# Performance work log

Measured on AMD Instinct MI355X. Metric: run time of the kernel, lower is better.

Reference implementation:

```python
import jax, jax.numpy as jnp
import numpy as np

D = 1024       # d_model
H = 16         # nhead
HD = D // H    # head_dim = 64
FF = 4096      # dim_feedforward
EPS = 1e-5


def layer_norm(x, gamma, beta, eps=EPS):
    mu = jnp.mean(x, axis=-1, keepdims=True)
    var = jnp.var(x, axis=-1, keepdims=True)
    return (x - mu) * jax.lax.rsqrt(var + eps) * gamma + beta


def setup_inputs() -> dict:
    key = jax.random.key(0)
    ks = jax.random.split(key, 12)
    rn = lambda k, shape, s=0.02: (jax.random.normal(k, shape, jnp.float32) * s)
    return {
        "src": jax.random.normal(ks[0], (4, 2048, D), jnp.float32),
        "Wqkv": rn(ks[1], (D, 3 * D)),          # qkv_proj weight (bias=False), stored (in,out)
        "Wout": rn(ks[2], (D, D)),              # out_proj weight (bias=False)
        "W1": rn(ks[3], (D, FF)),               # linear1
        "b1": jnp.zeros((FF,), jnp.float32),
        "W2": rn(ks[4], (FF, D)),               # linear2
        "b2": jnp.zeros((D,), jnp.float32),
        "g1": jnp.ones((D,), jnp.float32),      # norm1 weight
        "be1": jnp.zeros((D,), jnp.float32),    # norm1 bias
        "g2": jnp.ones((D,), jnp.float32),      # norm2 weight
        "be2": jnp.zeros((D,), jnp.float32),    # norm2 bias
    }


def reference(src, Wqkv, Wout, W1, b1, W2, b2, g1, be1, g2, be2):
    B, S, _ = src.shape
    # --- self attention (naive/MATH-backend SDPA, post-norm, eval: dropout=0) ---
    qkv = src @ Wqkv                                  # [B,S,3D]
    qkv = qkv.reshape(B, S, 3, H, HD)
    q = qkv[:, :, 0].transpose(0, 2, 1, 3)            # [B,H,S,HD]
    k = qkv[:, :, 1].transpose(0, 2, 1, 3)
    v = qkv[:, :, 2].transpose(0, 2, 1, 3)
    scores = jnp.einsum("bhqd,bhkd->bhqk", q, k) / np.float32(np.sqrt(HD))  # [B,H,S,S]
    attn = jax.nn.softmax(scores, axis=-1)
    ctx = jnp.einsum("bhqk,bhkd->bhqd", attn, v)      # [B,H,S,HD]
    ctx = ctx.transpose(0, 2, 1, 3).reshape(B, S, D)  # [B,S,D]
    attn_out = ctx @ Wout
    # residual + norm1
    x = layer_norm(src + attn_out, g1, be1)
    # --- FFN ---
    ff = jax.nn.relu(x @ W1 + b1) @ W2 + b2
    # residual + norm2
    return layer_norm(x + ff, g2, be2)
```

## Files before the change

### kernel.cpp

```cpp
#include <hip/hip_runtime.h>
#include <hip/hip_bf16.h>


typedef __attribute__((ext_vector_type(8))) short          short8;
typedef __attribute__((ext_vector_type(8))) unsigned short ushort8;
typedef __attribute__((ext_vector_type(4))) float          f32x4;
typedef __attribute__((ext_vector_type(2))) unsigned int   uivec2;

__device__ __forceinline__ unsigned short f2bf(float f) {
    union { float f; unsigned int u; } v; v.f = f;
    unsigned int u = v.u;
    unsigned int r = (u + 0x7fffu + ((u >> 16) & 1u)) >> 16;
    return (unsigned short)r;
}

__device__ __forceinline__ float bf2f(unsigned short u) {
    union { unsigned int u; float f; } v; v.u = ((unsigned int)u) << 16;
    return v.f;
}

__device__ __forceinline__ unsigned int pack_bf16_trunc(float lo, float hi) {
    union { float f; unsigned int u; } a, b; a.f = lo; b.f = hi;
    return __builtin_amdgcn_perm(b.u, a.u, 0x07060302u);
}

__device__ __forceinline__ void async_load16(const void* g, void* l) {
    __builtin_amdgcn_global_load_lds(
        (const __attribute__((address_space(1))) void*)(unsigned long long)g,
        (__attribute__((address_space(3))) void*)(unsigned long long)l,
        16, 0, 0);
}

__device__ __forceinline__ void softmax_frag(const f32x4* s,
                                             short8& pf0, short8& pf1) {
    unsigned int aw[4], bw[4];
#pragma unroll
    for (int nt = 0; nt < 4; nt++) {
        float p0 = __builtin_amdgcn_exp2f(s[nt][0]);
        float p1 = __builtin_amdgcn_exp2f(s[nt][1]);
        float p2 = __builtin_amdgcn_exp2f(s[nt][2]);
        float p3 = __builtin_amdgcn_exp2f(s[nt][3]);
        aw[nt] = pack_bf16_trunc(p0, p1);
        bw[nt] = pack_bf16_trunc(p2, p3);
    }
    uivec2 rA = __builtin_amdgcn_permlane32_swap(aw[0], aw[1], false, false);
    uivec2 sA = __builtin_amdgcn_permlane32_swap(aw[2], aw[3], false, false);
    uivec2 rB = __builtin_amdgcn_permlane32_swap(bw[0], bw[1], false, false);
    uivec2 sB = __builtin_amdgcn_permlane32_swap(bw[2], bw[3], false, false);
    uivec2 tA = __builtin_amdgcn_permlane16_swap(rA.x, rA.y, false, false);
    uivec2 uA = __builtin_amdgcn_permlane16_swap(sA.x, sA.y, false, false);
    uivec2 tB = __builtin_amdgcn_permlane16_swap(rB.x, rB.y, false, false);
    uivec2 uB = __builtin_amdgcn_permlane16_swap(sB.x, sB.y, false, false);
    union { unsigned int w[4]; short8 v; } P0, P1;
    P0.w[0] = tA.x; P0.w[1] = tB.x; P0.w[2] = tA.y; P0.w[3] = tB.y;
    P1.w[0] = uA.x; P1.w[1] = uB.x; P1.w[2] = uA.y; P1.w[3] = uB.y;
    pf0 = P0.v;
    pf1 = P1.v;
}

__device__ __forceinline__ void transpose_tile32(
    const float* __restrict__ W, unsigned short* __restrict__ Wt,
    int K, int N, int n0, int k0, float (*tile)[33]) {
    int tx = threadIdx.x & 31, ty = threadIdx.x >> 5;
#pragma unroll
    for (int i = 0; i < 32; i += 8)
        tile[ty + i][tx] = W[(size_t)(k0 + ty + i) * N + n0 + tx];
    __syncthreads();
#pragma unroll
    for (int i = 0; i < 32; i += 8)
        Wt[(size_t)(n0 + ty + i) * K + k0 + tx] = f2bf(tile[tx][ty + i]);
}

__global__ __launch_bounds__(256) void prep_kernel(
    const float* __restrict__ src, unsigned short* __restrict__ src_bf,
    const float* __restrict__ Wqkv, unsigned short* __restrict__ Wqkv_t,
    const float* __restrict__ Wout, unsigned short* __restrict__ Wout_t,
    const float* __restrict__ W1, unsigned short* __restrict__ W1_t,
    const float* __restrict__ W2, unsigned short* __restrict__ W2_t) {
    __shared__ float tile[32][33];
    const int bid = blockIdx.x;
    if (bid < 8192) {
        size_t i = ((size_t)bid * 256 + threadIdx.x) * 4;
        float4 v = *(const float4*)(src + i);
        ushort4 o;
        o.x = f2bf(v.x); o.y = f2bf(v.y); o.z = f2bf(v.z); o.w = f2bf(v.w);
        *(ushort4*)(src_bf + i) = o;
    } else if (bid < 11264) {
        int r = bid - 8192;
        transpose_tile32(Wqkv, Wqkv_t, 1024, 3072, (r % 96) * 32, (r / 96) * 32, tile);
    } else if (bid < 12288) {
        int r = bid - 11264;
        transpose_tile32(Wout, Wout_t, 1024, 1024, (r % 32) * 32, (r / 32) * 32, tile);
    } else if (bid < 16384) {
        int r = bid - 12288;
        transpose_tile32(W1, W1_t, 1024, 4096, (r % 128) * 32, (r / 128) * 32, tile);
    } else {
        int r = bid - 16384;
        transpose_tile32(W2, W2_t, 4096, 1024, (r % 32) * 32, (r / 32) * 32, tile);
    }
}

template <int MODE>
__global__ __launch_bounds__(256) void gemm_bf16_kernel(
    const unsigned short* __restrict__ A, const unsigned short* __restrict__ Bt,
    int M, int N, int K, int Kstride,
    float* __restrict__ outF, unsigned short* __restrict__ outB,
    const float* __restrict__ bias,
    const float* __restrict__ resF, const unsigned short* __restrict__ resB,
    unsigned short* __restrict__ vtB) {
    __shared__ unsigned short As[2][128 * 32];
    __shared__ unsigned short Bs[2][128 * 32];

    const int t = threadIdx.x;
    const int m0 = blockIdx.x * 128, n0 = blockIdx.y * 128;
    const int koff = blockIdx.z * K;
    const int wid = t >> 6, lane = t & 63;
    const int wm = wid >> 1, wn = wid & 1;
    const int lr = lane & 15, quad = lane >> 4;

    const int srow = lane >> 2;
    const int sch  = ((lane & 3) ^ (srow & 3)) * 8;
    const unsigned short* Ag =
        A  + (size_t)(m0 + wid * 32 + srow) * Kstride + koff + sch;
    const unsigned short* Bg =
        Bt + (size_t)(n0 + wid * 32 + srow) * Kstride + koff + sch;
    const int wofs = (wid * 32) * 32;
    const size_t rstep = (size_t)16 * Kstride;

    const int axs = ((quad ^ (lr & 3))) * 8;
    f32x4 acc[4][4] = {};

    const int nK = K >> 5;
    async_load16(Ag,         &As[0][wofs]);
    async_load16(Ag + rstep, &As[0][wofs + 16 * 32]);
    async_load16(Bg,         &Bs[0][wofs]);
    async_load16(Bg + rstep, &Bs[0][wofs + 16 * 32]);

    for (int kt = 0; kt < nK; kt++) {
        const int cur = kt & 1, nxt = cur ^ 1;
        __syncthreads();
        if (kt + 1 < nK) {
            const int k1 = (kt + 1) * 32;
            async_load16(Ag + k1,         &As[nxt][wofs]);
            async_load16(Ag + k1 + rstep, &As[nxt][wofs + 16 * 32]);
            async_load16(Bg + k1,         &Bs[nxt][wofs]);
            async_load16(Bg + k1 + rstep, &Bs[nxt][wofs + 16 * 32]);
        }

        short8 af[4], bfr[4];
#pragma unroll
        for (int i = 0; i < 4; i++) {
            af[i]  = *(const short8*)&As[cur][(wm * 64 + i * 16 + lr) * 32 + axs];
            bfr[i] = *(const short8*)&Bs[cur][(wn * 64 + i * 16 + lr) * 32 + axs];
        }
#pragma unroll
        for (int mi = 0; mi < 4; mi++)
#pragma unroll
            for (int ni = 0; ni < 4; ni++)
                acc[mi][ni] = __builtin_amdgcn_mfma_f32_16x16x32_bf16(
                    af[mi], bfr[ni], acc[mi][ni], 0, 0, 0);
    }

    const float QSC = 0.18033688011112042f;
#pragma unroll
    for (int mi = 0; mi < 4; mi++)
#pragma unroll
        for (int ni = 0; ni < 4; ni++) {
            const int col  = n0 + wn * 64 + ni * 16 + lr;
            const int row0 = m0 + wm * 64 + mi * 16 + quad * 4;
            if (MODE == 4 && col >= 2048) {
                int bb = row0 >> 11, ss = row0 & 2047, c = col - 2048;
                ushort4 ov;
                ov.x = f2bf(acc[mi][ni][0]); ov.y = f2bf(acc[mi][ni][1]);
                ov.z = f2bf(acc[mi][ni][2]); ov.w = f2bf(acc[mi][ni][3]);
                *(ushort4*)&vtB[((size_t)bb * 1024 + c) * 2048 + ss] = ov;
            } else {
#pragma unroll
                for (int r = 0; r < 4; r++) {
                    size_t idx = (size_t)(row0 + r) * N + col;
                    float v = acc[mi][ni][r];
                    if (MODE == 4) {
                        outB[idx] = f2bf(col < 1024 ? v * QSC : v);
                    } else if (MODE == 0) {
                        outB[idx] = f2bf(v);
                    } else if (MODE == 1) {
                        outF[idx] = v + resF[idx];
                    } else if (MODE == 2) {
                        v += bias[col];
                        outB[idx] = f2bf(v > 0.f ? v : 0.f);
                    } else if (MODE == 7) {
                        outB[idx] = f2bf(v + bf2f(resB[idx]));
                    } else if (MODE == 9) {
                        outB[idx] = f2bf(v + bias[col] + bf2f(resB[idx]));
                    }
                }
            }
        }
}

__global__ __launch_bounds__(256, 2) void attention_kernel(
    const unsigned short* __restrict__ qkv, const unsigned short* __restrict__ Vt,
    unsigned short* __restrict__ ctx) {
    __shared__ unsigned short Kbuf[2][64 * 64];
    __shared__ unsigned short Vbuf[2][64 * 64];

    const int qt = blockIdx.x, h = blockIdx.y, b = blockIdx.z;
    const int t = threadIdx.x, wid = t >> 6, lane = t & 63;
    const int lr = lane & 15, quad = lane >> 4;
    const int q0 = qt * 256 + wid * 64;

    short8 qf[4][2];
#pragma unroll
    for (int f = 0; f < 4; f++) {
        size_t qb = ((size_t)(b * 2048 + q0 + f * 16 + lr)) * 3072 + h * 64;
        qf[f][0] = *(const short8*)(qkv + qb + quad * 8);
        qf[f][1] = *(const short8*)(qkv + qb + 32 + quad * 8);
    }

    const int srow = wid * 8 + (lane >> 3);
    const int sch  = ((lane & 7) ^ (srow & 7)) * 8;
    const unsigned short* Kg =
        qkv + (size_t)b * 2048 * 3072 + 1024 + h * 64 + (size_t)srow * 3072 + sch;
    const unsigned short* Vg =
        Vt + ((size_t)b * 1024 + h * 64 + srow) * 2048 + sch;
    unsigned short* KsB = (unsigned short*)&Kbuf[0][(wid * 8) * 64];
    unsigned short* VsB = (unsigned short*)&Vbuf[0][(wid * 8) * 64];
    const int bufstep = 64 * 64;

    short8 ones;
#pragma unroll
    for (int i = 0; i < 8; i++) ones[i] = (short)0x3F80;

    f32x4 o[4][4] = {};
    f32x4 lacc[4] = {};

#pragma unroll
    for (int half = 0; half < 2; half++) {
        async_load16(Kg + (size_t)(half * 32) * 3072, KsB + half * 32 * 64);
        async_load16(Vg + (size_t)(half * 32) * 2048, VsB + half * 32 * 64);
    }

    const int swz = lr & 7;

    for (int kt = 0; kt < 32; kt++) {
        const int cur = kt & 1, nxt = cur ^ 1;
        __syncthreads();
        if (kt + 1 < 32) {
#pragma unroll
            for (int half = 0; half < 2; half++) {
                async_load16(Kg + (size_t)((kt + 1) * 64 + half * 32) * 3072,
                             KsB + nxt * bufstep + half * 32 * 64);
                async_load16(Vg + (size_t)(half * 32) * 2048 + (kt + 1) * 64,
                             VsB + nxt * bufstep + half * 32 * 64);
            }
        }

        const unsigned short* Kc = &Kbuf[cur][0];
        const unsigned short* Vc = &Vbuf[cur][0];

        f32x4 s[4][4] = {};
#pragma unroll
        for (int nt = 0; nt < 4; nt++) {
            const unsigned short* krow = Kc + (nt * 16 + lr) * 64;
            short8 kf0 = *(const short8*)(krow + (quad ^ swz) * 8);
            short8 kf1 = *(const short8*)(krow + ((quad + 4) ^ swz) * 8);
#pragma unroll
            for (int f = 0; f < 4; f++) {
                s[f][nt] = __builtin_amdgcn_mfma_f32_16x16x32_bf16(
                    kf0, qf[f][0], s[f][nt], 0, 0, 0);
                s[f][nt] = __builtin_amdgcn_mfma_f32_16x16x32_bf16(
                    kf1, qf[f][1], s[f][nt], 0, 0, 0);
            }
        }

        short8 pf[4][2];
#pragma unroll
        for (int f = 0; f < 4; f++)
            softmax_frag(s[f], pf[f][0], pf[f][1]);

#pragma unroll
        for (int nt = 0; nt < 4; nt++) {
            const unsigned short* vrow = Vc + (nt * 16 + lr) * 64;
            short8 vf0 = *(const short8*)(vrow + (quad ^ swz) * 8);
            short8 vf1 = *(const short8*)(vrow + ((quad + 4) ^ swz) * 8);
#pragma unroll
            for (int f = 0; f < 4; f++) {
                o[f][nt] = __builtin_amdgcn_mfma_f32_16x16x32_bf16(
                    pf[f][0], vf0, o[f][nt], 0, 0, 0);
                o[f][nt] = __builtin_amdgcn_mfma_f32_16x16x32_bf16(
                    pf[f][1], vf1, o[f][nt], 0, 0, 0);
            }
        }
#pragma unroll
        for (int f = 0; f < 4; f++) {
            lacc[f] = __builtin_amdgcn_mfma_f32_16x16x32_bf16(
                pf[f][0], ones, lacc[f], 0, 0, 0);
            lacc[f] = __builtin_amdgcn_mfma_f32_16x16x32_bf16(
                pf[f][1], ones, lacc[f], 0, 0, 0);
        }
    }

#pragma unroll
    for (int f = 0; f < 4; f++)
#pragma unroll
        for (int r = 0; r < 4; r++) {
            float li = 1.f / lacc[f][r];
            int q = q0 + f * 16 + quad * 4 + r;
#pragma unroll
            for (int nt = 0; nt < 4; nt++)
                ctx[((size_t)(b * 2048 + q)) * 1024 + h * 64 + nt * 16 + lr] =
                    f2bf(o[f][nt][r] * li);
        }
}

template <int OUTMODE>
__global__ __launch_bounds__(256) void layernorm_bf_kernel(
    const unsigned short* __restrict__ x, const float* __restrict__ g,
    const float* __restrict__ be, float* __restrict__ yF,
    unsigned short* __restrict__ yB) {
    const int row = blockIdx.x, t = threadIdx.x;
    ushort4 xb = *(const ushort4*)(x + (size_t)row * 1024 + t * 4);
    float4 v;
    v.x = bf2f(xb.x); v.y = bf2f(xb.y); v.z = bf2f(xb.z); v.w = bf2f(xb.w);
    float s  = v.x + v.y + v.z + v.w;
    float sq = v.x * v.x + v.y * v.y + v.z * v.z + v.w * v.w;
#pragma unroll
    for (int d = 1; d < 64; d <<= 1) {
        s  += __shfl_xor(s, d, 64);
        sq += __shfl_xor(sq, d, 64);
    }
    __shared__ float sh[8];
    int wid = t >> 6, lane = t & 63;
    if (lane == 0) { sh[wid] = s; sh[4 + wid] = sq; }
    __syncthreads();
    s  = sh[0] + sh[1] + sh[2] + sh[3];
    sq = sh[4] + sh[5] + sh[6] + sh[7];
    float mu  = s * (1.f / 1024.f);
    float var = sq * (1.f / 1024.f) - mu * mu;
    float rstd = rsqrtf(var + 1e-5f);
    float4 gv = *(const float4*)(g + t * 4);
    float4 bv = *(const float4*)(be + t * 4);
    float4 y;
    y.x = (v.x - mu) * rstd * gv.x + bv.x;
    y.y = (v.y - mu) * rstd * gv.y + bv.y;
    y.z = (v.z - mu) * rstd * gv.z + bv.z;
    y.w = (v.w - mu) * rstd * gv.w + bv.w;
    if (OUTMODE == 0) {
        *(float4*)(yF + (size_t)row * 1024 + t * 4) = y;
    } else {
        ushort4 o;
        o.x = f2bf(y.x); o.y = f2bf(y.y); o.z = f2bf(y.z); o.w = f2bf(y.w);
        *(ushort4*)(yB + (size_t)row * 1024 + t * 4) = o;
    }
}

extern "C" void kernel_launch(void* const* d_in, const int* in_sizes, int n_in,
                              void* d_out, int out_size, void* d_ws, size_t ws_size,
                              hipStream_t stream) {
    const float* src  = (const float*)d_in[0];
    const float* Wqkv = (const float*)d_in[1];
    const float* Wout = (const float*)d_in[2];
    const float* W1   = (const float*)d_in[3];
    const float* b1   = (const float*)d_in[4];
    const float* W2   = (const float*)d_in[5];
    const float* b2   = (const float*)d_in[6];
    const float* g1   = (const float*)d_in[7];
    const float* be1  = (const float*)d_in[8];
    const float* g2   = (const float*)d_in[9];
    const float* be2  = (const float*)d_in[10];
    float* out = (float*)d_out;

    const size_t NT = 8192;
    char* ws = (char*)d_ws;
    unsigned short* src_bf = (unsigned short*)ws; ws += NT * 1024 * 2;
    unsigned short* Wqkv_t = (unsigned short*)ws; ws += (size_t)3072 * 1024 * 2;
    unsigned short* Wout_t = (unsigned short*)ws; ws += (size_t)1024 * 1024 * 2;
    unsigned short* W1_t   = (unsigned short*)ws; ws += (size_t)4096 * 1024 * 2;
    unsigned short* W2_t   = (unsigned short*)ws; ws += (size_t)1024 * 4096 * 2;
    unsigned short* qkv_bf = (unsigned short*)ws; ws += NT * 3072 * 2;
    unsigned short* ctx_bf = (unsigned short*)ws; ws += NT * 1024 * 2;
    unsigned short* x1_bf  = (unsigned short*)ws; ws += NT * 1024 * 2;
    unsigned short* y1_bf  = (unsigned short*)ws; ws += NT * 1024 * 2;
    unsigned short* h_bf   = (unsigned short*)ws; ws += NT * 4096 * 2;
    unsigned short* Vt = h_bf;
    unsigned short* x2_bf = qkv_bf;

    prep_kernel<<<20480, 256, 0, stream>>>(
        src, src_bf, Wqkv, Wqkv_t, Wout, Wout_t, W1, W1_t, W2, W2_t);

    gemm_bf16_kernel<4><<<dim3(64, 24), 256, 0, stream>>>(
        src_bf, Wqkv_t, 8192, 3072, 1024, 1024,
        nullptr, qkv_bf, nullptr, nullptr, nullptr, Vt);
    attention_kernel<<<dim3(8, 16, 4), 256, 0, stream>>>(qkv_bf, Vt, ctx_bf);
    gemm_bf16_kernel<7><<<dim3(64, 8), 256, 0, stream>>>(
        ctx_bf, Wout_t, 8192, 1024, 1024, 1024,
        nullptr, x1_bf, nullptr, nullptr, src_bf, nullptr);
    layernorm_bf_kernel<1><<<8192, 256, 0, stream>>>(
        x1_bf, g1, be1, nullptr, y1_bf);
    gemm_bf16_kernel<2><<<dim3(64, 32), 256, 0, stream>>>(
        y1_bf, W1_t, 8192, 4096, 1024, 1024,
        nullptr, h_bf, b1, nullptr, nullptr, nullptr);
    gemm_bf16_kernel<9><<<dim3(64, 8), 256, 0, stream>>>(
        h_bf, W2_t, 8192, 1024, 4096, 4096,
        nullptr, x2_bf, b2, nullptr, y1_bf, nullptr);
    layernorm_bf_kernel<0><<<8192, 256, 0, stream>>>(
        x2_bf, g2, be2, out, nullptr);
}
```

Measured before the change: 461.4 us.

## Stage V-transpose epilogue through LDS and use 64x64 weight transpose tiles

The QKV GEMM epilogue for the V columns now writes bf16 accumulators into shared memory, then emits coalesced 16-byte rows of the transposed V buffer instead of scattered 8-byte stores. The prep kernel switches to 64x64 transpose tiles and 8-element src conversion per thread, which cuts the block count and widens stores. In exchange there are extra LDS traffic and barriers in the epilogue, and a larger shared tile in prep, which may lower occupancy.

```diff
diff --git a/kernel.cpp b/kernel.cpp
--- a/kernel.cpp
+++ b/kernel.cpp
@@ -58,16 +58,16 @@
     pf1 = P1.v;
 }
 
-__device__ __forceinline__ void transpose_tile32(
+__device__ __forceinline__ void transpose_tile64(
     const float* __restrict__ W, unsigned short* __restrict__ Wt,
-    int K, int N, int n0, int k0, float (*tile)[33]) {
-    int tx = threadIdx.x & 31, ty = threadIdx.x >> 5;
-#pragma unroll
-    for (int i = 0; i < 32; i += 8)
+    int K, int N, int n0, int k0, float (*tile)[65]) {
+    int tx = threadIdx.x & 63, ty = threadIdx.x >> 6;
+#pragma unroll
+    for (int i = 0; i < 64; i += 4)
         tile[ty + i][tx] = W[(size_t)(k0 + ty + i) * N + n0 + tx];
     __syncthreads();
 #pragma unroll
-    for (int i = 0; i < 32; i += 8)
+    for (int i = 0; i < 64; i += 4)
         Wt[(size_t)(n0 + ty + i) * K + k0 + tx] = f2bf(tile[tx][ty + i]);
 }
 
@@ -77,26 +77,28 @@
     const float* __restrict__ Wout, unsigned short* __restrict__ Wout_t,
     const float* __restrict__ W1, unsigned short* __restrict__ W1_t,
     const float* __restrict__ W2, unsigned short* __restrict__ W2_t) {
-    __shared__ float tile[32][33];
+    __shared__ float tile[64][65];
     const int bid = blockIdx.x;
-    if (bid < 8192) {
-        size_t i = ((size_t)bid * 256 + threadIdx.x) * 4;
-        float4 v = *(const float4*)(src + i);
-        ushort4 o;
-        o.x = f2bf(v.x); o.y = f2bf(v.y); o.z = f2bf(v.z); o.w = f2bf(v.w);
-        *(ushort4*)(src_bf + i) = o;
-    } else if (bid < 11264) {
-        int r = bid - 8192;
-        transpose_tile32(Wqkv, Wqkv_t, 1024, 3072, (r % 96) * 32, (r / 96) * 32, tile);
-    } else if (bid < 12288) {
-        int r = bid - 11264;
-        transpose_tile32(Wout, Wout_t, 1024, 1024, (r % 32) * 32, (r / 32) * 32, tile);
-    } else if (bid < 16384) {
-        int r = bid - 12288;
-        transpose_tile32(W1, W1_t, 1024, 4096, (r % 128) * 32, (r / 128) * 32, tile);
+    if (bid < 4096) {
+        size_t i = ((size_t)bid * 256 + threadIdx.x) * 8;
+        float4 v0 = *(const float4*)(src + i);
+        float4 v1 = *(const float4*)(src + i + 4);
+        ushort8 o;
+        o[0] = f2bf(v0.x); o[1] = f2bf(v0.y); o[2] = f2bf(v0.z); o[3] = f2bf(v0.w);
+        o[4] = f2bf(v1.x); o[5] = f2bf(v1.y); o[6] = f2bf(v1.z); o[7] = f2bf(v1.w);
+        *(ushort8*)(src_bf + i) = o;
+    } else if (bid < 4864) {
+        int r = bid - 4096;
+        transpose_tile64(Wqkv, Wqkv_t, 1024, 3072, (r % 48) * 64, (r / 48) * 64, tile);
+    } else if (bid < 5120) {
+        int r = bid - 4864;
+        transpose_tile64(Wout, Wout_t, 1024, 1024, (r % 16) * 64, (r / 16) * 64, tile);
+    } else if (bid < 6144) {
+        int r = bid - 5120;
+        transpose_tile64(W1, W1_t, 1024, 4096, (r % 64) * 64, (r / 64) * 64, tile);
     } else {
-        int r = bid - 16384;
-        transpose_tile32(W2, W2_t, 4096, 1024, (r % 32) * 32, (r / 32) * 32, tile);
+        int r = bid - 6144;
+        transpose_tile64(W2, W2_t, 4096, 1024, (r % 16) * 64, (r / 16) * 64, tile);
     }
 }
 
@@ -108,8 +110,9 @@
     const float* __restrict__ bias,
     const float* __restrict__ resF, const unsigned short* __restrict__ resB,
     unsigned short* __restrict__ vtB) {
-    __shared__ unsigned short As[2][128 * 32];
-    __shared__ unsigned short Bs[2][128 * 32];
+    __shared__ unsigned short Sh[4][128 * 32];
+    unsigned short (*As)[128 * 32] = &Sh[0];
+    unsigned short (*Bs)[128 * 32] = &Sh[2];
 
     const int t = threadIdx.x;
     const int m0 = blockIdx.x * 128, n0 = blockIdx.y * 128;
@@ -162,37 +165,57 @@
     }
 
     const float QSC = 0.18033688011112042f;
+
+    if (MODE == 4 && n0 >= 2048) {
+        unsigned short* T = &Sh[0][0];
+        __syncthreads();
+#pragma unroll
+        for (int mi = 0; mi < 4; mi++)
+#pragma unroll
+            for (int ni = 0; ni < 4; ni++) {
+                const int cl = wn * 64 + ni * 16 + lr;
+                const int s0 = wm * 64 + mi * 16 + quad * 4;
+                ushort4 ov;
+                ov.x = f2bf(acc[mi][ni][0]); ov.y = f2bf(acc[mi][ni][1]);
+                ov.z = f2bf(acc[mi][ni][2]); ov.w = f2bf(acc[mi][ni][3]);
+                *(ushort4*)&T[cl * 128 + s0] = ov;
+            }
+        __syncthreads();
+        const int bb = m0 >> 11, ss0 = m0 & 2047;
+        const int li = t & 15;
+#pragma unroll
+        for (int pass = 0; pass < 8; pass++) {
+            const int cl = (t >> 4) + pass * 16;
+            ushort8 vv = *(const ushort8*)&T[cl * 128 + li * 8];
+            *(ushort8*)&vtB[((size_t)bb * 1024 + (n0 - 2048 + cl)) * 2048 +
+                            ss0 + li * 8] = vv;
+        }
+        return;
+    }
+
 #pragma unroll
     for (int mi = 0; mi < 4; mi++)
 #pragma unroll
         for (int ni = 0; ni < 4; ni++) {
             const int col  = n0 + wn * 64 + ni * 16 + lr;
             const int row0 = m0 + wm * 64 + mi * 16 + quad * 4;
-            if (MODE == 4 && col >= 2048) {
-                int bb = row0 >> 11, ss = row0 & 2047, c = col - 2048;
-                ushort4 ov;
-                ov.x = f2bf(acc[mi][ni][0]); ov.y = f2bf(acc[mi][ni][1]);
-                ov.z = f2bf(acc[mi][ni][2]); ov.w = f2bf(acc[mi][ni][3]);
-                *(ushort4*)&vtB[((size_t)bb * 1024 + c) * 2048 + ss] = ov;
-            } else {
-#pragma unroll
-                for (int r = 0; r < 4; r++) {
-                    size_t idx = (size_t)(row0 + r) * N + col;
-                    float v = acc[mi][ni][r];
-                    if (MODE == 4) {
-                        outB[idx] = f2bf(col < 1024 ? v * QSC : v);
-                    } else if (MODE == 0) {
-                        outB[idx] = f2bf(v);
-                    } else if (MODE == 1) {
-                        outF[idx] = v + resF[idx];
-                    } else if (MODE == 2) {
-                        v += bias[col];
-                        outB[idx] = f2bf(v > 0.f ? v : 0.f);
-                    } else if (MODE == 7) {
-                        outB[idx] = f2bf(v + bf2f(resB[idx]));
-                    } else if (MODE == 9) {
-                        outB[idx] = f2bf(v + bias[col] + bf2f(resB[idx]));
-                    }
+#pragma unroll
+            for (int r = 0; r < 4; r++) {
+                size_t idx = (size_t)(row0 + r) * N + col;
+                float v = acc[mi][ni][r];
+                if (MODE == 4) {
+                    outB[idx] = f2bf(col < 1024 ? v * QSC : v);
+                } else if (MODE == 0) {
+                    outB[idx] = f2bf(v);
+                } else if (MODE == 1) {
+                    outF[idx] = v + resF[idx];
+                } else if (MODE == 2) {
+                    v += bias[col];
+                    outB[idx] = f2bf(v > 0.f ? v : 0.f);
+                } else if (MODE == 7) {
+                    outB[idx] = f2bf(v + bf2f(resB[idx]));
+                } else if (MODE == 9) {
+                    outB[idx] = f2bf(v + bias[col] + bf2f(resB[idx]));
                 }
             }
         }
@@ -385,7 +408,7 @@
     unsigned short* Vt = h_bf;
     unsigned short* x2_bf = qkv_bf;
 
-    prep_kernel<<<20480, 256, 0, stream>>>(
+    prep_kernel<<<7168, 256, 0, stream>>>(
         src, src_bf, Wqkv, Wqkv_t, Wout, Wout_t, W1, W1_t, W2, W2_t);
 
     gemm_bf16_kernel<4><<<dim3(64, 24), 256, 0, stream>>>(
```

New measurement: 480.8 us. 4.2% more time.
